# Kernel tuning notes

Hardware: AMD Instinct MI355X
Metric: run time of the kernel (lower is better)

Reference implementation:

```python
import jax, jax.numpy as jnp
import numpy as np

SEQ, BATCH, IN, HID = 2048, 16, 512, 512
QMAX = 127.0  # 8-bit narrow-range signed


def round_ste(x):
    # straight-through rounding (brevitas FloatToIntImplType.ROUND with STE)
    return x + jax.lax.stop_gradient(jnp.round(x) - x)


def weight_fake_quant(w, threshold):
    # scalar per-tensor scale = max|W| over concatenated [W_ri; W_rh], narrow-range int8
    s = threshold / QMAX
    return jnp.clip(round_ste(w / s), -QMAX, QMAX) * s


def act_fake_quant(x):
    # CONST scaling over [-1, 1], signed narrow-range int8 -> scale 1/127
    return jnp.clip(round_ste(x * QMAX), -QMAX, QMAX) / QMAX


def rnn_direction(inputs, w_ri, w_rh, b, reverse):
    threshold = jnp.maximum(jnp.max(jnp.abs(w_ri)), jnp.max(jnp.abs(w_rh)))
    q_ri = weight_fake_quant(w_ri, threshold)
    q_rh = weight_fake_quant(w_rh, threshold)
    xs = jnp.flip(inputs, 0) if reverse else inputs
    state0 = jnp.zeros((inputs.shape[1], w_rh.shape[0]), inputs.dtype)
    state0 = act_fake_quant(jnp.clip(state0, -1.0, 1.0))  # quant_input(state)

    def step(state, x_t):
        x_q = act_fake_quant(jnp.clip(x_t, -1.0, 1.0))  # QuantHardTanh on input
        gate = x_q @ q_ri + state @ q_rh + b            # [batch, hid]
        h = act_fake_quant(jnp.tanh(gate))              # QuantTanh
        return h, h

    _, outs = jax.lax.scan(step, state0, xs)            # [seq, batch, hid]
    return jnp.flip(outs, 0) if reverse else outs


def setup_inputs() -> dict:
    key = jax.random.key(0)
    ks = jax.random.split(key, 7)
    stdv = 1.0 / np.sqrt(HID)
    u = lambda k, shape: jax.random.uniform(k, shape, jnp.float32, -stdv, stdv)
    return {
        "inputs": jax.random.normal(ks[0], (SEQ, BATCH, IN), jnp.float32),
        "w_ri_f": u(ks[1], (IN, HID)),
        "w_rh_f": u(ks[2], (HID, HID)),
        "b_f": u(ks[3], (HID,)),
        "w_ri_b": u(ks[4], (IN, HID)),
        "w_rh_b": u(ks[5], (HID, HID)),
        "b_b": u(ks[6], (HID,)),
    }


def reference(inputs, w_ri_f, w_rh_f, b_f, w_ri_b, w_rh_b, b_b):
    out_f = rnn_direction(inputs, w_ri_f, w_rh_f, b_f, reverse=False)
    out_b = rnn_direction(inputs, w_ri_b, w_rh_b, b_b, reverse=True)
    return jnp.concatenate([out_f, out_b], axis=-1)  # [seq, batch, 2*hid]
```

## Files before the change

### kernel.cpp

```cpp
#include <hip/hip_runtime.h>
#include <stdint.h>

typedef int i32x4 __attribute__((ext_vector_type(4)));

#define TWO_LOG2E 2.8853900817779268f

#define WS_XQ_OFF   4096
#define XQ_BYTES    ((size_t)32768 * 512)
#define WRIT_BYTES  ((size_t)1024 * 512)
#define WRHT_BYTES  ((size_t)2 * 512 * 512)

__global__ __launch_bounds__(256) void k_absmax(const float* __restrict__ wri_f,
                                                const float* __restrict__ wrh_f,
                                                const float* __restrict__ wri_b,
                                                const float* __restrict__ wrh_b,
                                                unsigned* thrbits) {
    int dir = blockIdx.y;
    const float* a = dir ? wri_b : wri_f;
    const float* c = dir ? wrh_b : wrh_f;
    float m = 0.f;
    for (int i = blockIdx.x * 256 + threadIdx.x; i < 512 * 512; i += gridDim.x * 256) {
        m = fmaxf(m, fabsf(a[i]));
        m = fmaxf(m, fabsf(c[i]));
    }
    __shared__ float red[256];
    red[threadIdx.x] = m;
    __syncthreads();
    for (int s = 128; s > 0; s >>= 1) {
        if (threadIdx.x < s) red[threadIdx.x] = fmaxf(red[threadIdx.x], red[threadIdx.x + s]);
        __syncthreads();
    }
    if (threadIdx.x == 0) atomicMax(&thrbits[dir], __float_as_uint(red[0]));
}

__global__ __launch_bounds__(256) void k_quant_w(const float* __restrict__ wri_f,
                                                 const float* __restrict__ wrh_f,
                                                 const float* __restrict__ wri_b,
                                                 const float* __restrict__ wrh_b,
                                                 const unsigned* __restrict__ thrbits,
                                                 signed char* __restrict__ writ,
                                                 signed char* __restrict__ wrht) {
    int id = blockIdx.x;
    int dir = id & 1;
    int which = (id >> 1) & 1;
    int tile = id >> 2;
    int ti = tile >> 3, tj = tile & 7;
    const float* src = which ? (dir ? wrh_b : wrh_f) : (dir ? wri_b : wri_f);
    signed char* dst = which ? (wrht + (size_t)dir * 512 * 512) : (writ + (size_t)dir * 512 * 512);
    float s = __uint_as_float(thrbits[dir]) / 127.0f;
    __shared__ signed char t8[64][68];
    int tx = threadIdx.x & 63, ty = threadIdx.x >> 6;
    int i0 = ti * 64, j0 = tj * 64;
#pragma unroll
    for (int r = 0; r < 16; ++r) {
        int il = r * 4 + ty;
        float w = src[(size_t)(i0 + il) * 512 + j0 + tx];
        float q = rintf(w / s);
        q = fminf(fmaxf(q, -127.f), 127.f);
        t8[il][tx] = (signed char)(int)q;
    }
    __syncthreads();
#pragma unroll
    for (int r = 0; r < 16; ++r) {
        int jl = r * 4 + ty;
        dst[(size_t)(j0 + jl) * 512 + i0 + tx] = t8[tx][jl];
    }
}

__global__ __launch_bounds__(256) void k_quant_x(const float* __restrict__ x,
                                                 signed char* __restrict__ xq) {
    int i = blockIdx.x * 256 + threadIdx.x;
    float4 v = ((const float4*)x)[i];
    int q0 = (int)rintf(fminf(fmaxf(v.x, -1.f), 1.f) * 127.f);
    int q1 = (int)rintf(fminf(fmaxf(v.y, -1.f), 1.f) * 127.f);
    int q2 = (int)rintf(fminf(fmaxf(v.z, -1.f), 1.f) * 127.f);
    int q3 = (int)rintf(fminf(fmaxf(v.w, -1.f), 1.f) * 127.f);
    ((int*)xq)[i] = (q0 & 255) | ((q1 & 255) << 8) | ((q2 & 255) << 16) | ((q3 & 255) << 24);
}

__global__ __launch_bounds__(256, 2) void k_gemm_xif(const signed char* __restrict__ xq,
                                                     const signed char* __restrict__ writ,
                                                     const float* __restrict__ b_f,
                                                     const float* __restrict__ b_b,
                                                     const unsigned* __restrict__ thrbits,
                                                     float* __restrict__ out) {
    int bid = blockIdx.x;
    int mt8 = bid >> 3;
    int nt8 = bid & 7;
    int w = threadIdx.x >> 6, lane = threadIdx.x & 63;
    int l15 = lane & 15, q = lane >> 4;
    int M0 = mt8 * 128 + (w >> 1) * 64;
    int N0 = nt8 * 128 + (w & 1) * 64;
    int dir = N0 >> 9;
    float thr = __uint_as_float(thrbits[dir]);
    float gs2 = thr * (TWO_LOG2E / (127.f * 127.f));
    const float* bp = dir ? b_b : b_f;
    float bi2[4];
#pragma unroll
    for (int nt = 0; nt < 4; ++nt)
        bi2[nt] = bp[(N0 & 511) + nt * 16 + l15] * TWO_LOG2E;

    i32x4 acc[4][4];
#pragma unroll
    for (int mt = 0; mt < 4; ++mt)
#pragma unroll
        for (int nt = 0; nt < 4; ++nt)
            acc[mt][nt] = (i32x4){0, 0, 0, 0};

#pragma unroll
    for (int kb = 0; kb < 8; ++kb) {
        i32x4 af[4], bf[4];
#pragma unroll
        for (int mt = 0; mt < 4; ++mt)
            af[mt] = *(const i32x4*)(xq + (size_t)(M0 + mt * 16 + l15) * 512 + kb * 64 + q * 16);
#pragma unroll
        for (int nt = 0; nt < 4; ++nt)
            bf[nt] = *(const i32x4*)(writ + (size_t)(N0 + nt * 16 + l15) * 512 + kb * 64 + q * 16);
#pragma unroll
        for (int mt = 0; mt < 4; ++mt)
#pragma unroll
            for (int nt = 0; nt < 4; ++nt)
                acc[mt][nt] = __builtin_amdgcn_mfma_i32_16x16x64_i8(af[mt], bf[nt], acc[mt][nt], 0, 0, 0);
    }
#pragma unroll
    for (int mt = 0; mt < 4; ++mt)
#pragma unroll
        for (int nt = 0; nt < 4; ++nt)
#pragma unroll
            for (int r = 0; r < 4; ++r) {
                int row = M0 + mt * 16 + q * 4 + r;
                int col = N0 + nt * 16 + l15;
                out[(size_t)row * 1024 + col] = fmaf((float)acc[mt][nt][r], gs2, bi2[nt]);
            }
}

__global__ __launch_bounds__(512, 2) void k_rnn(const signed char* __restrict__ wrht,
                                                const unsigned* __restrict__ thrbits,
                                                float* __restrict__ out) {
    int bid = blockIdx.x;
    int dir = bid >> 4, batch = bid & 15;
    int w = threadIdx.x >> 6, lane = threadIdx.x & 63;
    int l15 = lane & 15, q = lane >> 4;
    int n0 = w * 64;
    float thr = __uint_as_float(thrbits[dir]);
    float gs2 = thr * (TWO_LOG2E / (127.f * 127.f));
    const signed char* wq = wrht + (size_t)dir * 512 * 512;

    i32x4 bf[8][4];
#pragma unroll
    for (int kb = 0; kb < 8; ++kb)
#pragma unroll
        for (int nt = 0; nt < 4; ++nt)
            bf[kb][nt] = *(const i32x4*)(wq + (size_t)(n0 + nt * 16 + l15) * 512 + kb * 64 + q * 16);

    __shared__ __align__(16) signed char st[2][16][528];
    for (int i = threadIdx.x; i < 2 * 16 * 528; i += 512) ((signed char*)st)[i] = 0;
    __syncthreads();

    int t0 = dir ? 2047 : 0;
    float xi[4], xin[4];
    size_t xrow0 = ((size_t)t0 * 16 + batch) * 1024 + (size_t)dir * 512;
#pragma unroll
    for (int nt = 0; nt < 4; ++nt) xi[nt] = out[xrow0 + n0 + nt * 16 + l15];

    int pp = 0;
    for (int step = 0; step < 2048; ++step) {
        int tcur = dir ? (2047 - step) : step;
        int nstep = (step + 1 < 2048) ? (step + 1) : step;
        int tnext = dir ? (2047 - nstep) : nstep;
        size_t xrowN = ((size_t)tnext * 16 + batch) * 1024 + (size_t)dir * 512;
#pragma unroll
        for (int nt = 0; nt < 4; ++nt) xin[nt] = out[xrowN + n0 + nt * 16 + l15];

        i32x4 af[8];
#pragma unroll
        for (int kb = 0; kb < 8; ++kb)
            af[kb] = *(const i32x4*)&st[pp][l15][kb * 64 + q * 16];

        float houtf[4];
        int hbyte[4];
#pragma unroll
        for (int nt = 0; nt < 4; ++nt) {
            i32x4 acc = (i32x4){0, 0, 0, 0};
#pragma unroll
            for (int kb = 0; kb < 8; ++kb)
                acc = __builtin_amdgcn_mfma_i32_16x16x64_i8(af[kb], bf[kb][nt], acc, 0, 0, 0);
            float arg = fmaf((float)acc[0], gs2, xi[nt]);
            float e = __builtin_amdgcn_exp2f(arg);
            float r = __builtin_amdgcn_rcpf(1.0f + e);
            float h127 = rintf(fmaf(r, -254.0f, 127.0f));
            houtf[nt] = h127 * (1.0f / 127.0f);
            hbyte[nt] = (int)h127;
        }

        size_t orow = ((size_t)tcur * 16 + batch) * 1024 + (size_t)dir * 512;
        if (lane < 16) {
#pragma unroll
            for (int nt = 0; nt < 4; ++nt) {
                out[orow + n0 + nt * 16 + lane] = houtf[nt];
                st[pp ^ 1][0][n0 + nt * 16 + lane] = (signed char)hbyte[nt];
            }
        }
#pragma unroll
        for (int nt = 0; nt < 4; ++nt) xi[nt] = xin[nt];
        __syncthreads();
        pp ^= 1;
    }
}

extern "C" void kernel_launch(void* const* d_in, const int* in_sizes, int n_in,
                              void* d_out, int out_size, void* d_ws, size_t ws_size,
                              hipStream_t stream) {
    const float* x     = (const float*)d_in[0];
    const float* wri_f = (const float*)d_in[1];
    const float* wrh_f = (const float*)d_in[2];
    const float* b_f   = (const float*)d_in[3];
    const float* wri_b = (const float*)d_in[4];
    const float* wrh_b = (const float*)d_in[5];
    const float* b_b   = (const float*)d_in[6];
    float* out = (float*)d_out;
    char* ws = (char*)d_ws;

    size_t need = WS_XQ_OFF + XQ_BYTES + WRIT_BYTES + WRHT_BYTES;
    if (ws_size < need) return;

    unsigned* thrbits = (unsigned*)ws;
    signed char* xq   = (signed char*)(ws + WS_XQ_OFF);
    signed char* writ = xq + XQ_BYTES;
    signed char* wrht = writ + WRIT_BYTES;

    hipMemsetAsync(thrbits, 0, 8, stream);
    k_absmax<<<dim3(64, 2), 256, 0, stream>>>(wri_f, wrh_f, wri_b, wrh_b, thrbits);
    k_quant_w<<<256, 256, 0, stream>>>(wri_f, wrh_f, wri_b, wrh_b, thrbits, writ, wrht);
    k_quant_x<<<16384, 256, 0, stream>>>(x, xq);
    k_gemm_xif<<<2048, 256, 0, stream>>>(xq, writ, b_f, b_b, thrbits, out);
    k_rnn<<<32, 512, 0, stream>>>(wrht, thrbits, out);
}
```

Baseline: 1.743 ms.

## Replace MFMA recurrent matvec with per-thread sdot4 dot products over LDS state

The recurrent step no longer pads the single batch row into a 16-row MFMA tile, which wasted most of each int8 MFMA. Instead each thread owns one hidden unit, keeps its 512 int8 weights in registers, and accumulates with sdot4 against state vectors broadcast from LDS. The full __syncthreads is replaced by an explicit lgkmcnt wait plus s_barrier, and pointer arithmetic is simplified. This trades matrix-core throughput for VALU dot products, 128 VGPRs of weights per thread, and 32 broadcast LDS reads per step.

```diff
diff --git a/kernel.cpp b/kernel.cpp
--- a/kernel.cpp
+++ b/kernel.cpp
@@ -9,6 +9,19 @@
 #define XQ_BYTES    ((size_t)32768 * 512)
 #define WRIT_BYTES  ((size_t)1024 * 512)
 #define WRHT_BYTES  ((size_t)2 * 512 * 512)
+
+static __device__ __forceinline__ int dot4(int a, int b, int c) {
+#if __has_builtin(__builtin_amdgcn_sdot4)
+    return __builtin_amdgcn_sdot4(a, b, c, false);
+#else
+    int r = c;
+    r += (int)(signed char)(a) * (int)(signed char)(b);
+    r += (int)(signed char)(a >> 8) * (int)(signed char)(b >> 8);
+    r += (int)(signed char)(a >> 16) * (int)(signed char)(b >> 16);
+    r += (int)(signed char)(a >> 24) * (int)(signed char)(b >> 24);
+    return r;
+#endif
+}
 
 __global__ __launch_bounds__(256) void k_absmax(const float* __restrict__ wri_f,
                                                 const float* __restrict__ wrh_f,
@@ -139,71 +152,53 @@
                                                 float* __restrict__ out) {
     int bid = blockIdx.x;
     int dir = bid >> 4, batch = bid & 15;
-    int w = threadIdx.x >> 6, lane = threadIdx.x & 63;
-    int l15 = lane & 15, q = lane >> 4;
-    int n0 = w * 64;
+    int n = threadIdx.x;
     float thr = __uint_as_float(thrbits[dir]);
     float gs2 = thr * (TWO_LOG2E / (127.f * 127.f));
-    const signed char* wq = wrht + (size_t)dir * 512 * 512;
-
-    i32x4 bf[8][4];
-#pragma unroll
-    for (int kb = 0; kb < 8; ++kb)
-#pragma unroll
-        for (int nt = 0; nt < 4; ++nt)
-            bf[kb][nt] = *(const i32x4*)(wq + (size_t)(n0 + nt * 16 + l15) * 512 + kb * 64 + q * 16);
-
-    __shared__ __align__(16) signed char st[2][16][528];
-    for (int i = threadIdx.x; i < 2 * 16 * 528; i += 512) ((signed char*)st)[i] = 0;
+    const signed char* wq = wrht + (size_t)dir * 512 * 512 + (size_t)n * 512;
+
+    i32x4 w[32];
+#pragma unroll
+    for (int i = 0; i < 32; ++i)
+        w[i] = *(const i32x4*)(wq + i * 16);
+
+    __shared__ __align__(16) signed char st[2][512];
+    if (threadIdx.x < 256) ((int*)st)[threadIdx.x] = 0;
     __syncthreads();
 
     int t0 = dir ? 2047 : 0;
-    float xi[4], xin[4];
-    size_t xrow0 = ((size_t)t0 * 16 + batch) * 1024 + (size_t)dir * 512;
-#pragma unroll
-    for (int nt = 0; nt < 4; ++nt) xi[nt] = out[xrow0 + n0 + nt * 16 + l15];
-
+    const long long rowstride = (long long)(dir ? -1 : 1) * 16 * 1024;
+    float* prow = out + (size_t)t0 * 16 * 1024 + (size_t)batch * 1024 + (size_t)dir * 512 + n;
+
+    float xi = *prow;
     int pp = 0;
     for (int step = 0; step < 2048; ++step) {
-        int tcur = dir ? (2047 - step) : step;
-        int nstep = (step + 1 < 2048) ? (step + 1) : step;
-        int tnext = dir ? (2047 - nstep) : nstep;
-        size_t xrowN = ((size_t)tnext * 16 + batch) * 1024 + (size_t)dir * 512;
-#pragma unroll
-        for (int nt = 0; nt < 4; ++nt) xin[nt] = out[xrowN + n0 + nt * 16 + l15];
-
-        i32x4 af[8];
-#pragma unroll
-        for (int kb = 0; kb < 8; ++kb)
-            af[kb] = *(const i32x4*)&st[pp][l15][kb * 64 + q * 16];
-
-        float houtf[4];
-        int hbyte[4];
-#pragma unroll
-        for (int nt = 0; nt < 4; ++nt) {
-            i32x4 acc = (i32x4){0, 0, 0, 0};
-#pragma unroll
-            for (int kb = 0; kb < 8; ++kb)
-                acc = __builtin_amdgcn_mfma_i32_16x16x64_i8(af[kb], bf[kb][nt], acc, 0, 0, 0);
-            float arg = fmaf((float)acc[0], gs2, xi[nt]);
-            float e = __builtin_amdgcn_exp2f(arg);
-            float r = __builtin_amdgcn_rcpf(1.0f + e);
-            float h127 = rintf(fmaf(r, -254.0f, 127.0f));
-            houtf[nt] = h127 * (1.0f / 127.0f);
-            hbyte[nt] = (int)h127;
+        float* pnext = prow + ((step + 1 < 2048) ? rowstride : 0);
+        float xin = *pnext;
+
+        int acc0 = 0, acc1 = 0, acc2 = 0, acc3 = 0;
+#pragma unroll
+        for (int kb = 0; kb < 32; ++kb) {
+            i32x4 s4 = *(const i32x4*)&st[pp][kb * 16];
+            acc0 = dot4(w[kb][0], s4[0], acc0);
+            acc1 = dot4(w[kb][1], s4[1], acc1);
+            acc2 = dot4(w[kb][2], s4[2], acc2);
+            acc3 = dot4(w[kb][3], s4[3], acc3);
         }
-
-        size_t orow = ((size_t)tcur * 16 + batch) * 1024 + (size_t)dir * 512;
-        if (lane < 16) {
-#pragma unroll
-            for (int nt = 0; nt < 4; ++nt) {
-                out[orow + n0 + nt * 16 + lane] = houtf[nt];
-                st[pp ^ 1][0][n0 + nt * 16 + lane] = (signed char)hbyte[nt];
-            }
-        }
-#pragma unroll
-        for (int nt = 0; nt < 4; ++nt) xi[nt] = xin[nt];
-        __syncthreads();
+        int acc = (acc0 + acc1) + (acc2 + acc3);
+
+        float arg = fmaf((float)acc, gs2, xi);
+        float e = __builtin_amdgcn_exp2f(arg);
+        float r = __builtin_amdgcn_rcpf(1.0f + e);
+        float h127 = rintf(fmaf(r, -254.0f, 127.0f));
+        *prow = h127 * (1.0f / 127.0f);
+        st[pp ^ 1][n] = (signed char)(int)h127;
+
+        xi = xin;
+        prow = pnext;
+        asm volatile("s_waitcnt lgkmcnt(0)" ::: "memory");
+        __builtin_amdgcn_s_barrier();
+        __builtin_amdgcn_sched_barrier(0);
         pp ^= 1;
     }
 }
```

New measurement: 1.622 ms. 6.9% less time.

## Process all batches per direction in one RNN block using transposed MFMA

Applied to the files above, without the earlier changes.

The recurrent kernel used to launch one block per (direction, batch) and run 16x16 MFMAs with only one useful batch row. It now launches one block per direction and treats all 16 batch rows as the MFMA N dimension, with weights as the A operand held in registers. Each lane reads and writes four contiguous hidden outputs as a float4 and stores packed int8 state. A magic-number float trick replaces rintf, and the full __syncthreads is replaced by an explicit waitcnt plus s_barrier. This removes the redundant matrix work and uses only two workgroups, so the sequential chain runs on two CUs instead of thirty-two.

```diff
diff --git a/kernel.cpp b/kernel.cpp
--- a/kernel.cpp
+++ b/kernel.cpp
@@ -2,6 +2,7 @@
 #include <stdint.h>
 
 typedef int i32x4 __attribute__((ext_vector_type(4)));
+typedef float f32x4 __attribute__((ext_vector_type(4)));
 
 #define TWO_LOG2E 2.8853900817779268f
 
@@ -137,8 +138,7 @@
 __global__ __launch_bounds__(512, 2) void k_rnn(const signed char* __restrict__ wrht,
                                                 const unsigned* __restrict__ thrbits,
                                                 float* __restrict__ out) {
-    int bid = blockIdx.x;
-    int dir = bid >> 4, batch = bid & 15;
+    int dir = blockIdx.x;
     int w = threadIdx.x >> 6, lane = threadIdx.x & 63;
     int l15 = lane & 15, q = lane >> 4;
     int n0 = w * 64;
@@ -146,64 +146,71 @@
     float gs2 = thr * (TWO_LOG2E / (127.f * 127.f));
     const signed char* wq = wrht + (size_t)dir * 512 * 512;
 
-    i32x4 bf[8][4];
-#pragma unroll
-    for (int kb = 0; kb < 8; ++kb)
-#pragma unroll
-        for (int nt = 0; nt < 4; ++nt)
-            bf[kb][nt] = *(const i32x4*)(wq + (size_t)(n0 + nt * 16 + l15) * 512 + kb * 64 + q * 16);
+    i32x4 a[4][8];
+#pragma unroll
+    for (int mt = 0; mt < 4; ++mt)
+#pragma unroll
+        for (int kb = 0; kb < 8; ++kb)
+            a[mt][kb] = *(const i32x4*)(wq + (size_t)(n0 + mt * 16 + l15) * 512 + kb * 64 + q * 16);
 
     __shared__ __align__(16) signed char st[2][16][528];
-    for (int i = threadIdx.x; i < 2 * 16 * 528; i += 512) ((signed char*)st)[i] = 0;
+    for (int i = threadIdx.x; i < 2 * 16 * 528 / 4; i += 512) ((int*)st)[i] = 0;
     __syncthreads();
 
+    const int rs = 16 * 1024;
     int t0 = dir ? 2047 : 0;
-    float xi[4], xin[4];
-    size_t xrow0 = ((size_t)t0 * 16 + batch) * 1024 + (size_t)dir * 512;
-#pragma unroll
-    for (int nt = 0; nt < 4; ++nt) xi[nt] = out[xrow0 + n0 + nt * 16 + l15];
+    int tstep = dir ? -rs : rs;
+    float* pbase = out + ((size_t)t0 * 16 + l15) * 1024 + dir * 512 + n0 + q * 4;
+
+    f32x4 xi[4];
+#pragma unroll
+    for (int mt = 0; mt < 4; ++mt) xi[mt] = *(const f32x4*)(pbase + mt * 16);
 
     int pp = 0;
     for (int step = 0; step < 2048; ++step) {
-        int tcur = dir ? (2047 - step) : step;
-        int nstep = (step + 1 < 2048) ? (step + 1) : step;
-        int tnext = dir ? (2047 - nstep) : nstep;
-        size_t xrowN = ((size_t)tnext * 16 + batch) * 1024 + (size_t)dir * 512;
-#pragma unroll
-        for (int nt = 0; nt < 4; ++nt) xin[nt] = out[xrowN + n0 + nt * 16 + l15];
-
-        i32x4 af[8];
+        float* pnext = pbase + ((step + 1 < 2048) ? tstep : 0);
+        f32x4 xin[4];
+#pragma unroll
+        for (int mt = 0; mt < 4; ++mt) xin[mt] = *(const f32x4*)(pnext + mt * 16);
+
+        i32x4 bf[8];
 #pragma unroll
         for (int kb = 0; kb < 8; ++kb)
-            af[kb] = *(const i32x4*)&st[pp][l15][kb * 64 + q * 16];
-
-        float houtf[4];
-        int hbyte[4];
-#pragma unroll
-        for (int nt = 0; nt < 4; ++nt) {
-            i32x4 acc = (i32x4){0, 0, 0, 0};
-#pragma unroll
-            for (int kb = 0; kb < 8; ++kb)
-                acc = __builtin_amdgcn_mfma_i32_16x16x64_i8(af[kb], bf[kb][nt], acc, 0, 0, 0);
-            float arg = fmaf((float)acc[0], gs2, xi[nt]);
-            float e = __builtin_amdgcn_exp2f(arg);
-            float r = __builtin_amdgcn_rcpf(1.0f + e);
-            float h127 = rintf(fmaf(r, -254.0f, 127.0f));
-            houtf[nt] = h127 * (1.0f / 127.0f);
-            hbyte[nt] = (int)h127;
+            bf[kb] = *(const i32x4*)&st[pp][l15][kb * 64 + q * 16];
+
+        i32x4 acc[4];
+#pragma unroll
+        for (int mt = 0; mt < 4; ++mt) acc[mt] = (i32x4){0, 0, 0, 0};
+#pragma unroll
+        for (int kb = 0; kb < 8; ++kb)
+#pragma unroll
+            for (int mt = 0; mt < 4; ++mt)
+                acc[mt] = __builtin_amdgcn_mfma_i32_16x16x64_i8(a[mt][kb], bf[kb], acc[mt], 0, 0, 0);
+
+#pragma unroll
+        for (int mt = 0; mt < 4; ++mt) {
+            unsigned packed = 0;
+            f32x4 ho;
+#pragma unroll
+            for (int r = 0; r < 4; ++r) {
+                float arg = fmaf((float)acc[mt][r], gs2, xi[mt][r]);
+                float e = __builtin_amdgcn_exp2f(arg);
+                float rc = __builtin_amdgcn_rcpf(1.0f + e);
+                float t = fmaf(rc, -254.0f, 127.0f);
+                float mm = t + 12582912.0f;
+                packed |= (__float_as_uint(mm) & 0xFFu) << (8 * r);
+                ho[r] = (mm - 12582912.0f) * (1.0f / 127.0f);
+            }
+            *(f32x4*)(pbase + mt * 16) = ho;
+            *(unsigned*)&st[pp ^ 1][l15][n0 + mt * 16 + q * 4] = packed;
         }
 
-        size_t orow = ((size_t)tcur * 16 + batch) * 1024 + (size_t)dir * 512;
-        if (lane < 16) {
-#pragma unroll
-            for (int nt = 0; nt < 4; ++nt) {
-                out[orow + n0 + nt * 16 + lane] = houtf[nt];
-                st[pp ^ 1][0][n0 + nt * 16 + lane] = (signed char)hbyte[nt];
-            }
-        }
-#pragma unroll
-        for (int nt = 0; nt < 4; ++nt) xi[nt] = xin[nt];
-        __syncthreads();
+#pragma unroll
+        for (int mt = 0; mt < 4; ++mt) xi[mt] = xin[mt];
+        pbase = pnext;
+        asm volatile("s_waitcnt lgkmcnt(0)" ::: "memory");
+        __builtin_amdgcn_s_barrier();
+        __builtin_amdgcn_sched_barrier(0);
         pp ^= 1;
     }
 }
@@ -234,5 +241,5 @@
     k_quant_w<<<256, 256, 0, stream>>>(wri_f, wrh_f, wri_b, wrh_b, thrbits, writ, wrht);
     k_quant_x<<<16384, 256, 0, stream>>>(x, xq);
     k_gemm_xif<<<2048, 256, 0, stream>>>(xq, writ, b_f, b_b, thrbits, out);
-    k_rnn<<<32, 512, 0, stream>>>(wrht, thrbits, out);
-}
+    k_rnn<<<2, 512, 0, stream>>>(wrht, thrbits, out);
+}
```

Result: slower. 3.969 ms (+127.7%).
